# Kernel optimization log

Hardware: AMD Instinct MI355X
Metric: run time of the kernel (lower is better)

The kernel has to match this reference:

```python
import jax, jax.numpy as jnp
import numpy as np

B, S, D_IN, HID, H = 4, 2048, 1024, 1024, 16
DH = HID // H


def setup_inputs() -> dict:
    key = jax.random.key(0)
    ks = jax.random.split(key, 10)
    s = 0.02
    return {
        "x": jax.random.normal(ks[0], (B, S, D_IN), dtype=jnp.float32),
        "Wq": jax.random.normal(ks[1], (D_IN, HID), dtype=jnp.float32) * s,
        "bq": jnp.zeros((HID,), dtype=jnp.float32),
        "Wk": jax.random.normal(ks[2], (D_IN, HID), dtype=jnp.float32) * s,
        "bk": jnp.zeros((HID,), dtype=jnp.float32),
        "Wv": jax.random.normal(ks[3], (D_IN, HID), dtype=jnp.float32) * s,
        "bv": jnp.zeros((HID,), dtype=jnp.float32),
        "Wo": jax.random.normal(ks[4], (HID, HID), dtype=jnp.float32) * s,
        "bo": jnp.zeros((HID,), dtype=jnp.float32),
        "padding_mask": jax.random.randint(ks[5], (B, S), 0, 2, dtype=jnp.int32),
    }


def reference(x, Wq, bq, Wk, bk, Wv, bv, Wo, bo, padding_mask):
    b, s, _ = x.shape
    q = (x @ Wq + bq).reshape(b, s, H, DH)  # [b, s, h, dh]
    k = (x @ Wk + bk).reshape(b, s, H, DH)
    v = (x @ Wv + bv).reshape(b, s, H, DH)

    # ALiBi: symmetric |i-j| distance bias, per-head slopes 2^{-m}
    r = jnp.arange(s)
    pos = jnp.abs(r[None, :] - r[:, None]).astype(jnp.float32)  # [s, s]
    step = 8.0 / H
    slopes = jnp.power(2.0, -jnp.arange(step, 8.0 + step, step, dtype=jnp.float32))  # [h]
    alibi = slopes[:, None, None] * pos[None, :, :]  # [h, s, s]

    scale = jnp.sqrt(jnp.float32(DH))
    attn = jnp.einsum("bqhd,bkhd->bhqk", q, k)
    attn = (attn - alibi[None]) / scale
    attn = jnp.where(padding_mask[:, None, None, :] == 0, -jnp.inf, attn)
    p = jax.nn.softmax(attn, axis=-1)

    out = jnp.einsum("bhqk,bkhd->bqhd", p, v).reshape(b, s, HID)
    return out @ Wo + bo
```

## Files before the change

### kernel.cpp

```cpp
#include <hip/hip_runtime.h>
#include <stdint.h>

#define NB     4
#define SEQ    2048
#define NH     16
#define DHD    64
#define DM     1024
#define MTOT   (NB*SEQ)
#define HSZ    (SEQ*DHD)

typedef __attribute__((ext_vector_type(8))) short bf16x8;
typedef __attribute__((ext_vector_type(4))) float f32x4;

__device__ __forceinline__ short f2bf(float f) {
  uint32_t u = __float_as_uint(f);
  u = (u + 0x7FFFu + ((u >> 16) & 1u)) >> 16;
  return (short)u;
}

__device__ __forceinline__ uint32_t cvtpk(float lo, float hi) {
  uint32_t r;
  asm("v_cvt_pk_bf16_f32 %0, %1, %2" : "=v"(r) : "v"(lo), "v"(hi));
  return r;
}

__device__ __forceinline__ float exp2a(float x) {
  float r;
  asm("v_exp_f32 %0, %1" : "=v"(r) : "v"(x));
  return r;
}

__device__ __forceinline__ float max3f(float a, float b, float c) {
  return fmaxf(fmaxf(a, b), c);
}

__device__ __forceinline__ f32x4 mfma16(bf16x8 a, bf16x8 b, f32x4 c) {
  return __builtin_amdgcn_mfma_f32_16x16x32_bf16(a, b, c, 0, 0, 0);
}

__device__ __forceinline__ void async16(const void* g, void* l) {
  __builtin_amdgcn_global_load_lds(
      (const __attribute__((address_space(1))) void*)g,
      (__attribute__((address_space(3))) void*)l, 16, 0, 0);
}

__global__ void k_cast(const float* __restrict__ in, short* __restrict__ out, int n) {
  int i = (blockIdx.x * blockDim.x + threadIdx.x) * 8;
  if (i >= n) return;
  float4 a = *reinterpret_cast<const float4*>(in + i);
  float4 b = *reinterpret_cast<const float4*>(in + i + 4);
  bf16x8 v;
  v[0] = f2bf(a.x); v[1] = f2bf(a.y); v[2] = f2bf(a.z); v[3] = f2bf(a.w);
  v[4] = f2bf(b.x); v[5] = f2bf(b.y); v[6] = f2bf(b.z); v[7] = f2bf(b.w);
  *reinterpret_cast<bf16x8*>(out + i) = v;
}

__global__ void k_maskbias(const int* __restrict__ pm, float* __restrict__ fb, int n) {
  int i = blockIdx.x * blockDim.x + threadIdx.x;
  if (i < n) fb[i] = pm[i] ? 0.0f : -1e30f;
}

__global__ void k_transpose(const float* __restrict__ in, short* __restrict__ out) {
  __shared__ float tile[32][33];
  int n0 = blockIdx.x * 32, k0 = blockIdx.y * 32;
  int tx = threadIdx.x, ty = threadIdx.y;
  #pragma unroll
  for (int i = 0; i < 32; i += 8)
    tile[ty + i][tx] = in[(size_t)(k0 + ty + i) * DM + n0 + tx];
  __syncthreads();
  #pragma unroll
  for (int i = 0; i < 32; i += 8)
    out[(size_t)(n0 + ty + i) * DM + k0 + tx] = f2bf(tile[tx][ty + i]);
}

template<int MODE>
__global__ void __launch_bounds__(256) k_gemm(const short* __restrict__ A,
                                              const short* __restrict__ Bt,
                                              const float* __restrict__ bias,
                                              void* __restrict__ Cv, float scale) {
  __shared__ short lA[128 * 32];
  __shared__ short lB[128 * 32];
  int lin = blockIdx.y * gridDim.x + blockIdx.x;
  int s = ((lin & 7) << 6) | (lin >> 3);
  int m0 = (s & 63) * 128, n0 = (s >> 6) * 128;
  int tid = threadIdx.x, lane = tid & 63, w = tid >> 6;
  int wr = w >> 1, wc = w & 1;
  int l15 = lane & 15, lg = lane >> 4;
  f32x4 acc[4][4] = {};

  int r0 = tid >> 2, c0 = (tid & 3) * 8;
  int r1 = (tid + 256) >> 2, c1 = ((tid + 256) & 3) * 8;
  const short* ga0 = A + (size_t)(m0 + r0) * DM + c0;
  const short* ga1 = A + (size_t)(m0 + r1) * DM + c1;
  const short* gb0 = Bt + (size_t)(n0 + r0) * DM + c0;
  const short* gb1 = Bt + (size_t)(n0 + r1) * DM + c1;
  short* lA0 = lA + w * 512;
  short* lA1 = lA + 2048 + w * 512;
  short* lB0 = lB + w * 512;
  short* lB1 = lB + 2048 + w * 512;

  for (int k0 = 0; k0 < DM; k0 += 32) {
    async16(ga0 + k0, lA0);
    async16(ga1 + k0, lA1);
    async16(gb0 + k0, lB0);
    async16(gb1 + k0, lB1);
    __syncthreads();
    bf16x8 af[4], bfr[4];
    #pragma unroll
    for (int i = 0; i < 4; ++i) {
      af[i]  = *reinterpret_cast<const bf16x8*>(lA + (wr * 64 + i * 16 + l15) * 32 + lg * 8);
      bfr[i] = *reinterpret_cast<const bf16x8*>(lB + (wc * 64 + i * 16 + l15) * 32 + lg * 8);
    }
    #pragma unroll
    for (int i = 0; i < 4; ++i)
      #pragma unroll
      for (int j = 0; j < 4; ++j)
        acc[i][j] = mfma16(af[i], bfr[j], acc[i][j]);
    __syncthreads();
  }

  #pragma unroll
  for (int j = 0; j < 4; ++j) {
    int cg = n0 + wc * 64 + j * 16 + l15;
    float bv = bias[cg];
    #pragma unroll
    for (int i = 0; i < 4; ++i) {
      #pragma unroll
      for (int r = 0; r < 4; ++r) {
        int rg = m0 + wr * 64 + i * 16 + lg * 4 + r;
        float val = (acc[i][j][r] + bv) * scale;
        if (MODE == 0) {
          ((short*)Cv)[(size_t)rg * DM + cg] = f2bf(val);
        } else if (MODE == 1) {
          int bh2 = ((rg >> 11) << 4) | (cg >> 6);
          int dh = cg & 63, sl = rg & 2047;
          size_t fi = (size_t)bh2 * HSZ + (size_t)(sl >> 6) * 4096
                    + (size_t)((((dh >> 4) * 8 + ((sl >> 3) & 7)) * 16 + (dh & 15)) * 8 + (sl & 7));
          ((short*)Cv)[fi] = f2bf(val);
        } else if (MODE == 3) {
          int bh2 = ((rg >> 11) << 4) | (cg >> 6);
          int dh = cg & 63, sl = rg & 2047;
          size_t fi = (size_t)bh2 * HSZ + (size_t)(sl >> 4) * 1024
                    + (size_t)((((dh >> 3) * 16 + (sl & 15)) * 8) + (dh & 7));
          ((short*)Cv)[fi] = f2bf(val);
        } else {
          ((float*)Cv)[(size_t)rg * DM + cg] = val;
        }
      }
    }
  }
}

__device__ __forceinline__ void softmax_half(const f32x4* st, const float4* fb4,
                                             float c2, float d0, int lg,
                                             float& mrun, float& ssum,
                                             f32x4* acc, uint32_t* wb) {
  float l[16];
  #pragma unroll
  for (int t = 0; t < 4; ++t) {
    l[t * 4 + 0] = fmaf(-c2, fabsf(d0 - (float)(t * 16 + 0)), st[t][0] + fb4[t].x);
    l[t * 4 + 1] = fmaf(-c2, fabsf(d0 - (float)(t * 16 + 1)), st[t][1] + fb4[t].y);
    l[t * 4 + 2] = fmaf(-c2, fabsf(d0 - (float)(t * 16 + 2)), st[t][2] + fb4[t].z);
    l[t * 4 + 3] = fmaf(-c2, fabsf(d0 - (float)(t * 16 + 3)), st[t][3] + fb4[t].w);
  }
  float ma = max3f(l[0], l[1], l[2]);
  float mb = max3f(l[3], l[4], l[5]);
  float mc = max3f(l[6], l[7], l[8]);
  float md = max3f(l[9], l[10], l[11]);
  float me = max3f(l[12], l[13], l[14]);
  float tmax = fmaxf(max3f(ma, mb, mc), max3f(md, me, l[15]));
  tmax = fmaxf(tmax, __shfl_xor(tmax, 16));
  tmax = fmaxf(tmax, __shfl_xor(tmax, 32));

  if (!__all(tmax <= mrun + 8.0f)) {
    float mn = fmaxf(mrun, tmax);
    float fsc = exp2a(mrun - mn);
    mrun = mn;
    ssum *= fsc;
    #pragma unroll
    for (int td = 0; td < 4; ++td) acc[td] *= fsc;
  }

  float p[16];
  #pragma unroll
  for (int i = 0; i < 16; ++i) p[i] = exp2a(l[i] - mrun);
  float a0 = p[0] + p[1],  a1 = p[2] + p[3],  a2 = p[4] + p[5],  a3 = p[6] + p[7];
  float a4 = p[8] + p[9],  a5 = p[10] + p[11], a6 = p[12] + p[13], a7 = p[14] + p[15];
  float b0 = a0 + a1, b1 = a2 + a3, b2 = a4 + a5, b3 = a6 + a7;
  float rs = (b0 + b1) + (b2 + b3);
  rs += __shfl_xor(rs, 16);
  rs += __shfl_xor(rs, 32);
  ssum += rs;

  #pragma unroll
  for (int t = 0; t < 4; ++t) {
    uint2 wv = { cvtpk(p[t * 4 + 0], p[t * 4 + 1]), cvtpk(p[t * 4 + 2], p[t * 4 + 3]) };
    *reinterpret_cast<uint2*>(wb + t * 8 + lg * 2) = wv;
  }
}

__global__ void __launch_bounds__(64, 3) k_attn(const short* __restrict__ Q,
                                                const short* __restrict__ KF,
                                                const short* __restrict__ VF,
                                                const float* __restrict__ fbias,
                                                short* __restrict__ O) {
  __shared__ uint32_t pbuf[2 * 16 * 38];
  int g = blockIdx.x;
  int qb = (g >> 3) & 63;
  int bh = (g & 7) + ((g >> 9) << 3);
  int b = bh >> 4, h = bh & 15;
  int lane = threadIdx.x;
  int l15 = lane & 15, lg = lane >> 4;
  int q0 = qb * 32;
  float c2 = exp2f(-0.5f * (float)(h + 1)) * 0.125f * 1.44269504f;

  const short* qpA = Q + (size_t)(b * SEQ + q0 + l15) * DM + h * DHD + lg * 8;
  bf16x8 bqA0 = *reinterpret_cast<const bf16x8*>(qpA);
  bf16x8 bqA1 = *reinterpret_cast<const bf16x8*>(qpA + 32);
  const short* qpB = qpA + (size_t)16 * DM;
  bf16x8 bqB0 = *reinterpret_cast<const bf16x8*>(qpB);
  bf16x8 bqB1 = *reinterpret_cast<const bf16x8*>(qpB + 32);

  const short* kbase = KF + (size_t)bh * HSZ + lane * 8;
  const short* vbase = VF + (size_t)bh * HSZ + lane * 8;
  const float* fb = fbias + b * SEQ;
  uint32_t* wbA = pbuf + l15 * 38;
  uint32_t* wbB = pbuf + 608 + l15 * 38;

  float mrunA = -1e30f, ssumA = 0.0f, mrunB = -1e30f, ssumB = 0.0f;
  f32x4 accA[4] = {}, accB[4] = {};
  float d0A = (float)(q0 + l15) - (float)(lg * 4);
  float d0B = d0A + 16.0f;

  for (int kt = 0; kt < SEQ; kt += 64) {
    float4 fb4[4];
    #pragma unroll
    for (int t = 0; t < 4; ++t)
      fb4[t] = *reinterpret_cast<const float4*>(fb + kt + t * 16 + lg * 4);

    const short* kp = kbase + (size_t)(kt >> 4) * 1024;
    bf16x8 ka[4][2];
    #pragma unroll
    for (int t = 0; t < 4; ++t) {
      ka[t][0] = *reinterpret_cast<const bf16x8*>(kp + t * 1024);
      ka[t][1] = *reinterpret_cast<const bf16x8*>(kp + t * 1024 + 512);
    }
    const short* vp = vbase + (size_t)(kt >> 6) * 4096;
    bf16x8 va[4][2];
    #pragma unroll
    for (int td = 0; td < 4; ++td) {
      va[td][0] = *reinterpret_cast<const bf16x8*>(vp + (td * 8 + 0) * 128);
      va[td][1] = *reinterpret_cast<const bf16x8*>(vp + (td * 8 + 4) * 128);
    }

    f32x4 stA[4], stB[4];
    __builtin_amdgcn_s_setprio(1);
    #pragma unroll
    for (int t = 0; t < 4; ++t) {
      f32x4 zA = {};
      zA = mfma16(ka[t][0], bqA0, zA);
      stA[t] = mfma16(ka[t][1], bqA1, zA);
      f32x4 zB = {};
      zB = mfma16(ka[t][0], bqB0, zB);
      stB[t] = mfma16(ka[t][1], bqB1, zB);
    }
    __builtin_amdgcn_s_setprio(0);

    softmax_half(stA, fb4, c2, d0A, lg, mrunA, ssumA, accA, wbA);
    softmax_half(stB, fb4, c2, d0B, lg, mrunB, ssumB, accB, wbB);

    asm volatile("s_waitcnt lgkmcnt(0)" ::: "memory");
    __builtin_amdgcn_sched_barrier(0);

    __builtin_amdgcn_s_setprio(1);
    #pragma unroll
    for (int ks = 0; ks < 2; ++ks) {
      int t = ks * 2 + (lg >> 1);
      bf16x8 pfA = *reinterpret_cast<const bf16x8*>(wbA + t * 8 + (lg & 1) * 4);
      bf16x8 pfB = *reinterpret_cast<const bf16x8*>(wbB + t * 8 + (lg & 1) * 4);
      #pragma unroll
      for (int td = 0; td < 4; ++td) {
        accA[td] = mfma16(va[td][ks], pfA, accA[td]);
        accB[td] = mfma16(va[td][ks], pfB, accB[td]);
      }
    }
    __builtin_amdgcn_s_setprio(0);
    d0A -= 64.0f; d0B -= 64.0f;
  }

  float invA = 1.0f / ssumA;
  float invB = 1.0f / ssumB;
  short* opA = O + (size_t)(b * SEQ + q0 + l15) * DM + h * DHD;
  short* opB = opA + (size_t)16 * DM;
  #pragma unroll
  for (int td = 0; td < 4; ++td) {
    uint2 wvA = { cvtpk(accA[td][0] * invA, accA[td][1] * invA),
                  cvtpk(accA[td][2] * invA, accA[td][3] * invA) };
    *reinterpret_cast<uint2*>(opA + td * 16 + lg * 4) = wvA;
    uint2 wvB = { cvtpk(accB[td][0] * invB, accB[td][1] * invB),
                  cvtpk(accB[td][2] * invB, accB[td][3] * invB) };
    *reinterpret_cast<uint2*>(opB + td * 16 + lg * 4) = wvB;
  }
}

extern "C" void kernel_launch(void* const* d_in, const int* in_sizes, int n_in,
                              void* d_out, int out_size, void* d_ws, size_t ws_size,
                              hipStream_t stream) {
  const float* x  = (const float*)d_in[0];
  const float* Wq = (const float*)d_in[1];
  const float* bq = (const float*)d_in[2];
  const float* Wk = (const float*)d_in[3];
  const float* bk = (const float*)d_in[4];
  const float* Wv = (const float*)d_in[5];
  const float* bv = (const float*)d_in[6];
  const float* Wo = (const float*)d_in[7];
  const float* bo = (const float*)d_in[8];
  const int*   pm = (const int*)d_in[9];

  char* ws = (char*)d_ws;
  const size_t MB = 1ull << 20;
  short* xb  = (short*)(ws + 0 * MB);
  short* q   = (short*)(ws + 16 * MB);
  short* kf  = (short*)(ws + 32 * MB);
  short* vf  = (short*)(ws + 48 * MB);
  short* ob  = (short*)(ws + 64 * MB);
  short* wqt = (short*)(ws + 80 * MB);
  short* wkt = (short*)(ws + 82 * MB);
  short* wvt = (short*)(ws + 84 * MB);
  short* wot = (short*)(ws + 86 * MB);
  float* fbias = (float*)(ws + 88 * MB);

  k_cast<<<dim3(MTOT * DM / 8 / 256), dim3(256), 0, stream>>>(x, xb, MTOT * DM);
  k_maskbias<<<dim3(MTOT / 256), dim3(256), 0, stream>>>(pm, fbias, MTOT);
  k_transpose<<<dim3(32, 32), dim3(32, 8), 0, stream>>>(Wq, wqt);
  k_transpose<<<dim3(32, 32), dim3(32, 8), 0, stream>>>(Wk, wkt);
  k_transpose<<<dim3(32, 32), dim3(32, 8), 0, stream>>>(Wv, wvt);
  k_transpose<<<dim3(32, 32), dim3(32, 8), 0, stream>>>(Wo, wot);
  k_gemm<0><<<dim3(64, 8), dim3(256), 0, stream>>>(xb, wqt, bq, q, 0.125f * 1.44269504f);
  k_gemm<3><<<dim3(64, 8), dim3(256), 0, stream>>>(xb, wkt, bk, kf, 1.0f);
  k_gemm<1><<<dim3(64, 8), dim3(256), 0, stream>>>(xb, wvt, bv, vf, 1.0f);
  k_attn<<<dim3(SEQ / 32 * NB * NH), dim3(64), 0, stream>>>(q, kf, vf, fbias, ob);
  k_gemm<2><<<dim3(64, 8), dim3(256), 0, stream>>>(ob, wot, bo, d_out, 1.0f);
}
```

Baseline: 260.0 us.

## Process 64 query rows per attention wave to reuse K/V loads

Each single-wave attention block now handles four 16-row query sub-tiles (64 rows) instead of two, so every K and V fragment loaded from global memory feeds twice as many MFMAs. The grid halves accordingly and the block index decode is adjusted. Launch bounds drop to one wave per SIMD hint, and register pressure rises from the larger accumulator set, which may lower occupancy and latency hiding. The LDS probability buffer doubles to hold all four sub-tiles.

```diff
diff --git a/kernel.cpp b/kernel.cpp
--- a/kernel.cpp
+++ b/kernel.cpp
@@ -199,38 +199,43 @@
   }
 }
 
-__global__ void __launch_bounds__(64, 3) k_attn(const short* __restrict__ Q,
+__global__ void __launch_bounds__(64, 1) k_attn(const short* __restrict__ Q,
                                                 const short* __restrict__ KF,
                                                 const short* __restrict__ VF,
                                                 const float* __restrict__ fbias,
                                                 short* __restrict__ O) {
-  __shared__ uint32_t pbuf[2 * 16 * 38];
+  __shared__ uint32_t pbuf[4 * 16 * 38];
   int g = blockIdx.x;
-  int qb = (g >> 3) & 63;
-  int bh = (g & 7) + ((g >> 9) << 3);
+  int qb = (g >> 3) & 31;
+  int bh = (g & 7) + ((g >> 8) << 3);
   int b = bh >> 4, h = bh & 15;
   int lane = threadIdx.x;
   int l15 = lane & 15, lg = lane >> 4;
-  int q0 = qb * 32;
+  int q0 = qb * 64;
   float c2 = exp2f(-0.5f * (float)(h + 1)) * 0.125f * 1.44269504f;
 
-  const short* qpA = Q + (size_t)(b * SEQ + q0 + l15) * DM + h * DHD + lg * 8;
-  bf16x8 bqA0 = *reinterpret_cast<const bf16x8*>(qpA);
-  bf16x8 bqA1 = *reinterpret_cast<const bf16x8*>(qpA + 32);
-  const short* qpB = qpA + (size_t)16 * DM;
-  bf16x8 bqB0 = *reinterpret_cast<const bf16x8*>(qpB);
-  bf16x8 bqB1 = *reinterpret_cast<const bf16x8*>(qpB + 32);
+  const short* qp0 = Q + (size_t)(b * SEQ + q0 + l15) * DM + h * DHD + lg * 8;
+  bf16x8 bq[4][2];
+  #pragma unroll
+  for (int hh = 0; hh < 4; ++hh) {
+    bq[hh][0] = *reinterpret_cast<const bf16x8*>(qp0 + (size_t)(hh * 16) * DM);
+    bq[hh][1] = *reinterpret_cast<const bf16x8*>(qp0 + (size_t)(hh * 16) * DM + 32);
+  }
 
   const short* kbase = KF + (size_t)bh * HSZ + lane * 8;
   const short* vbase = VF + (size_t)bh * HSZ + lane * 8;
   const float* fb = fbias + b * SEQ;
-  uint32_t* wbA = pbuf + l15 * 38;
-  uint32_t* wbB = pbuf + 608 + l15 * 38;
-
-  float mrunA = -1e30f, ssumA = 0.0f, mrunB = -1e30f, ssumB = 0.0f;
-  f32x4 accA[4] = {}, accB[4] = {};
-  float d0A = (float)(q0 + l15) - (float)(lg * 4);
-  float d0B = d0A + 16.0f;
+  uint32_t* wb[4];
+  #pragma unroll
+  for (int hh = 0; hh < 4; ++hh) wb[hh] = pbuf + hh * 608 + l15 * 38;
+
+  float mrun[4], ssum[4], d0[4];
+  f32x4 acc[4][4] = {};
+  #pragma unroll
+  for (int hh = 0; hh < 4; ++hh) {
+    mrun[hh] = -1e30f; ssum[hh] = 0.0f;
+    d0[hh] = (float)(q0 + hh * 16 + l15) - (float)(lg * 4);
+  }
 
   for (int kt = 0; kt < SEQ; kt += 64) {
     float4 fb4[4];
@@ -253,21 +258,20 @@
       va[td][1] = *reinterpret_cast<const bf16x8*>(vp + (td * 8 + 4) * 128);
     }
 
-    f32x4 stA[4], stB[4];
-    __builtin_amdgcn_s_setprio(1);
-    #pragma unroll
-    for (int t = 0; t < 4; ++t) {
-      f32x4 zA = {};
-      zA = mfma16(ka[t][0], bqA0, zA);
-      stA[t] = mfma16(ka[t][1], bqA1, zA);
-      f32x4 zB = {};
-      zB = mfma16(ka[t][0], bqB0, zB);
-      stB[t] = mfma16(ka[t][1], bqB1, zB);
-    }
-    __builtin_amdgcn_s_setprio(0);
-
-    softmax_half(stA, fb4, c2, d0A, lg, mrunA, ssumA, accA, wbA);
-    softmax_half(stB, fb4, c2, d0B, lg, mrunB, ssumB, accB, wbB);
+    #pragma unroll
+    for (int hh = 0; hh < 4; ++hh) {
+      f32x4 st[4];
+      __builtin_amdgcn_s_setprio(1);
+      #pragma unroll
+      for (int t = 0; t < 4; ++t) {
+        f32x4 z = {};
+        z = mfma16(ka[t][0], bq[hh][0], z);
+        st[t] = mfma16(ka[t][1], bq[hh][1], z);
+      }
+      __builtin_amdgcn_s_setprio(0);
+      softmax_half(st, fb4, c2, d0[hh], lg, mrun[hh], ssum[hh], acc[hh], wb[hh]);
+      d0[hh] -= 64.0f;
+    }
 
     asm volatile("s_waitcnt lgkmcnt(0)" ::: "memory");
     __builtin_amdgcn_sched_barrier(0);
@@ -276,30 +280,29 @@
     #pragma unroll
     for (int ks = 0; ks < 2; ++ks) {
       int t = ks * 2 + (lg >> 1);
-      bf16x8 pfA = *reinterpret_cast<const bf16x8*>(wbA + t * 8 + (lg & 1) * 4);
-      bf16x8 pfB = *reinterpret_cast<const bf16x8*>(wbB + t * 8 + (lg & 1) * 4);
-      #pragma unroll
-      for (int td = 0; td < 4; ++td) {
-        accA[td] = mfma16(va[td][ks], pfA, accA[td]);
-        accB[td] = mfma16(va[td][ks], pfB, accB[td]);
-      }
+      bf16x8 pf[4];
+      #pragma unroll
+      for (int hh = 0; hh < 4; ++hh)
+        pf[hh] = *reinterpret_cast<const bf16x8*>(wb[hh] + t * 8 + (lg & 1) * 4);
+      #pragma unroll
+      for (int td = 0; td < 4; ++td)
+        #pragma unroll
+        for (int hh = 0; hh < 4; ++hh)
+          acc[hh][td] = mfma16(va[td][ks], pf[hh], acc[hh][td]);
     }
     __builtin_amdgcn_s_setprio(0);
-    d0A -= 64.0f; d0B -= 64.0f;
-  }
-
-  float invA = 1.0f / ssumA;
-  float invB = 1.0f / ssumB;
-  short* opA = O + (size_t)(b * SEQ + q0 + l15) * DM + h * DHD;
-  short* opB = opA + (size_t)16 * DM;
-  #pragma unroll
-  for (int td = 0; td < 4; ++td) {
-    uint2 wvA = { cvtpk(accA[td][0] * invA, accA[td][1] * invA),
-                  cvtpk(accA[td][2] * invA, accA[td][3] * invA) };
-    *reinterpret_cast<uint2*>(opA + td * 16 + lg * 4) = wvA;
-    uint2 wvB = { cvtpk(accB[td][0] * invB, accB[td][1] * invB),
-                  cvtpk(accB[td][2] * invB, accB[td][3] * invB) };
-    *reinterpret_cast<uint2*>(opB + td * 16 + lg * 4) = wvB;
+  }
+
+  #pragma unroll
+  for (int hh = 0; hh < 4; ++hh) {
+    float inv = 1.0f / ssum[hh];
+    short* op = O + (size_t)(b * SEQ + q0 + hh * 16 + l15) * DM + h * DHD;
+    #pragma unroll
+    for (int td = 0; td < 4; ++td) {
+      uint2 wv = { cvtpk(acc[hh][td][0] * inv, acc[hh][td][1] * inv),
+                   cvtpk(acc[hh][td][2] * inv, acc[hh][td][3] * inv) };
+      *reinterpret_cast<uint2*>(op + td * 16 + lg * 4) = wv;
+    }
   }
 }
 
@@ -339,6 +342,6 @@
   k_gemm<0><<<dim3(64, 8), dim3(256), 0, stream>>>(xb, wqt, bq, q, 0.125f * 1.44269504f);
   k_gemm<3><<<dim3(64, 8), dim3(256), 0, stream>>>(xb, wkt, bk, kf, 1.0f);
   k_gemm<1><<<dim3(64, 8), dim3(256), 0, stream>>>(xb, wvt, bv, vf, 1.0f);
-  k_attn<<<dim3(SEQ / 32 * NB * NH), dim3(64), 0, stream>>>(q, kf, vf, fbias, ob);
+  k_attn<<<dim3(SEQ / 64 * NB * NH), dim3(64), 0, stream>>>(q, kf, vf, fbias, ob);
   k_gemm<2><<<dim3(64, 8), dim3(256), 0, stream>>>(ob, wot, bo, d_out, 1.0f);
 }
```

Result: slower. 333.5 us (+28.3%).
